# Performance work log

Hardware: AMD Instinct MI355X
Metric: run time of the kernel (lower is better)

## Reference

```python
import jax, jax.numpy as jnp
import numpy as np

S = 256          # fine grid extent (active region within full_scale=4096)
SC = S // 2      # coarse grid extent after stride-2 downsample
N = 400_000      # active fine voxels
C_IN, M0, M1 = 3, 32, 64   # input features; unet_structure = [32, 64]
NCLASS = 20
EPS = 1e-4       # scn.BatchNormReLU default eps


def _build_nbr(keys_sorted, coords, s):
    """27-neighborhood index table for a sparse voxel set (hash via sorted keys)."""
    n = coords.shape[0]
    nbr = np.full((n, 27), -1, dtype=np.int32)
    x, y, z = coords[:, 0], coords[:, 1], coords[:, 2]
    k = 0
    for dx in (-1, 0, 1):
        for dy in (-1, 0, 1):
            for dz in (-1, 0, 1):
                nx, ny, nz = x + dx, y + dy, z + dz
                valid = (nx >= 0) & (nx < s) & (ny >= 0) & (ny < s) & (nz >= 0) & (nz < s)
                ck = (nx.astype(np.int64) * s + ny) * s + nz
                pos = np.clip(np.searchsorted(keys_sorted, ck), 0, n - 1)
                nbr[:, k] = np.where(valid & (keys_sorted[pos] == ck), pos, -1)
                k += 1
    return nbr


def setup_inputs() -> dict:
    rng = np.random.default_rng(0)
    keys = np.sort(rng.choice(S ** 3, size=N, replace=False).astype(np.int64))
    x = keys // (S * S); y = (keys // S) % S; z = keys % S
    coords = np.stack([x, y, z], 1)
    nbr_fine = _build_nbr(keys, coords, S)
    # stride-2 pooling structure
    ckeys = ((x // 2) * SC + (y // 2)) * SC + (z // 2)
    uk, parent_id = np.unique(ckeys, return_inverse=True)
    ccoords = np.stack([uk // (SC * SC), (uk // SC) % SC, uk % SC], 1)
    nbr_coarse = _build_nbr(uk, ccoords, SC)
    child_off = ((x & 1) * 4 + (y & 1) * 2 + (z & 1)).astype(np.int32)

    ks = jax.random.split(jax.random.key(0), 16)
    def w(k, shape, fan_in):
        return jax.random.normal(k, shape, jnp.float32) * (1.0 / np.sqrt(fan_in))
    return {
        "feats": jax.random.normal(ks[0], (N, C_IN), jnp.float32),
        "nbr_fine": jnp.asarray(nbr_fine),
        "nbr_coarse": jnp.asarray(nbr_coarse),
        "parent_id": jnp.asarray(parent_id.astype(np.int32)),
        "child_off": jnp.asarray(child_off),
        "W_sub": w(ks[1], (27, C_IN, M0), 27 * C_IN),
        "W_e0": w(ks[2], (27, M0, M0), 27 * M0),
        "g0": jnp.ones((M0,), jnp.float32), "b0": jnp.zeros((M0,), jnp.float32),
        "W_down": w(ks[3], (8, M0, M1), 8 * M0),
        "W_e1": w(ks[4], (27, M1, M1), 27 * M1),
        "g1": jnp.ones((M1,), jnp.float32), "b1": jnp.zeros((M1,), jnp.float32),
        "W_up": w(ks[5], (8, M1, M0), 8 * M1),
        "W_dec": w(ks[6], (27, 2 * M0, M0), 27 * 2 * M0),
        "g_out": jnp.ones((M0,), jnp.float32), "b_out": jnp.zeros((M0,), jnp.float32),
        "W_lin": w(ks[7], (M0, NCLASS), M0),
        "b_lin": jnp.zeros((NCLASS,), jnp.float32),
    }


def _subconv(feat, nbr, W):
    """Submanifold 3x3x3 conv: fixed loop over 27 kernel taps (gather+GEMM)."""
    out = jnp.zeros((feat.shape[0], W.shape[2]), feat.dtype)
    for k in range(27):
        idx = nbr[:, k]
        g = jnp.where(idx[:, None] >= 0, feat[jnp.clip(idx, 0)], 0.0)
        out = out + g @ W[k]
    return out


def _bnrelu(xv, g, b):
    mu = xv.mean(0)
    var = xv.var(0)
    return jax.nn.relu((xv - mu) * jax.lax.rsqrt(var + EPS) * g + b)


def reference(feats, nbr_fine, nbr_coarse, parent_id, child_off,
              W_sub, W_e0, g0, b0, W_down, W_e1, g1, b1, W_up, W_dec,
              g_out, b_out, W_lin, b_lin):
    M = nbr_coarse.shape[0]
    xv = _subconv(feats, nbr_fine, W_sub)                       # [N, M0]
    e0 = _bnrelu(_subconv(xv, nbr_fine, W_e0), g0, b0)          # encoder level 0
    # stride-2 sparse conv (scatter-add children into parents, per-offset weight)
    down = jax.ops.segment_sum(jnp.einsum('nc,ncd->nd', e0, W_down[child_off]),
                               parent_id, num_segments=M)        # [M, M1]
    e1 = _bnrelu(_subconv(down, nbr_coarse, W_e1), g1, b1)      # encoder level 1
    # stride-2 sparse deconv (gather parent, per-offset weight)
    up = jnp.einsum('nc,ncd->nd', e1[parent_id], W_up[child_off])  # [N, M0]
    dec = _subconv(jnp.concatenate([e0, up], 1), nbr_fine, W_dec)  # decoder join
    feature = _bnrelu(dec, g_out, b_out)                        # final BatchNormReLU
    y = feature @ W_lin + b_lin                                 # class head
    return (y, feature)
```

## Files before the change

kernel.cpp:

```cpp
#include <hip/hip_runtime.h>
#include <hip/hip_bf16.h>

#define BN_EPS 1e-4f

typedef __attribute__((ext_vector_type(8))) short short8;
typedef __attribute__((ext_vector_type(4))) float float4e;

__device__ __forceinline__ int rfl(int x) { return __builtin_amdgcn_readfirstlane(x); }

__device__ __forceinline__ float ldf(const __hip_bfloat16* p) { return __bfloat162float(*p); }
__device__ __forceinline__ void stf(__hip_bfloat16* p, float v) { *p = __float2bfloat16(v); }

__device__ __forceinline__ short bfbits(float x) {
    __hip_bfloat16 h = __float2bfloat16(x);
    short s;
    __builtin_memcpy(&s, &h, 2);
    return s;
}
__device__ __forceinline__ short8 cvt8(float4 a, float4 b) {
    short8 r;
    r[0] = bfbits(a.x); r[1] = bfbits(a.y); r[2] = bfbits(a.z); r[3] = bfbits(a.w);
    r[4] = bfbits(b.x); r[5] = bfbits(b.y); r[6] = bfbits(b.z); r[7] = bfbits(b.w);
    return r;
}

__global__ __launch_bounds__(256) void k_pack(const float* __restrict__ src,
                                              __hip_bfloat16* __restrict__ dst,
                                              int CIN, int COUT, int KT, int NT, int total) {
    int i = blockIdx.x * 256 + threadIdx.x;
    if (i >= total) return;
    int j = i & 7, lane = (i >> 3) & 63;
    int g = i >> 9;
    int nt = g % NT; g /= NT;
    int kt = g % KT; g /= KT;
    int t = g;
    int q = lane >> 4, c = lane & 15;
    dst[i] = __float2bfloat16(src[((size_t)t * CIN + kt * 32 + q * 8 + j) * COUT + nt * 16 + c]);
}

__global__ __launch_bounds__(256) void k_xv(const float* __restrict__ feats,
                                            const int* __restrict__ nbr,
                                            const float* __restrict__ W,
                                            __hip_bfloat16* __restrict__ out, int N) {
    int n = blockIdx.x * 256 + threadIdx.x;
    if (n >= N) return;
    float acc[32];
#pragma unroll
    for (int d = 0; d < 32; ++d) acc[d] = 0.f;
    const int* nb = nbr + (size_t)n * 27;
    for (int k = 0; k < 27; ++k) {
        int idx = nb[k];
        if (idx < 0) continue;
        float f0 = feats[(size_t)idx * 3 + 0];
        float f1 = feats[(size_t)idx * 3 + 1];
        float f2 = feats[(size_t)idx * 3 + 2];
        const float* w = W + k * 96;
#pragma unroll
        for (int d = 0; d < 32; ++d)
            acc[d] += f0 * w[d] + f1 * w[32 + d] + f2 * w[64 + d];
    }
    short8* o = (short8*)(out + (size_t)n * 32);
#pragma unroll
    for (int c = 0; c < 4; ++c) {
        short8 r;
#pragma unroll
        for (int j = 0; j < 8; ++j) r[j] = bfbits(acc[c * 8 + j]);
        o[c] = r;
    }
}

template <int CIN, int COUT, int MODE>
__global__ __launch_bounds__(256, 4) void k_conv(const void* __restrict__ inAv,
                                                 const void* __restrict__ inBv,
                                                 const int* __restrict__ nbr,
                                                 const __hip_bfloat16* __restrict__ Wp,
                                                 __hip_bfloat16* __restrict__ out,
                                                 int nrows,
                                                 float* __restrict__ ssum,
                                                 float* __restrict__ ssq) {
    constexpr int KT = CIN / 32;
    constexpr int NT = COUT / 16;
    __shared__ int sidx[4][432];
    const __hip_bfloat16* inAb = (const __hip_bfloat16*)inAv;
    const __hip_bfloat16* inBb = (const __hip_bfloat16*)inBv;
    const float* inAf = (const float*)inAv;
    const int tid = threadIdx.x;
    const int lane = tid & 63;
    const int wv = tid >> 6;
    const int m15 = lane & 15;
    const int q = lane >> 4;
    int* my = sidx[wv];
    int wid = blockIdx.x * 4 + wv;
    int nw = gridDim.x * 4;
    const int ntile = (nrows + 15) / 16;
    float sS[NT], sQ[NT];
#pragma unroll
    for (int nt = 0; nt < NT; ++nt) { sS[nt] = 0.f; sQ[nt] = 0.f; }

    for (int tile = wid; tile < ntile; tile += nw) {
        const int row0 = rfl(tile) * 16;
        int nr = nrows - row0;
        nr = nr > 16 ? 16 : nr;
        const int* src = nbr + (size_t)row0 * 27;
        const int tot = nr * 27;
        for (int t = lane; t < 432; t += 64) {
            int v = -1;
            if (t < tot) v = src[t];
            int r = t / 27;
            my[(t - r * 27) * 16 + r] = v;
        }
        float4e acc[NT];
#pragma unroll
        for (int nt = 0; nt < NT; ++nt) acc[nt] = (float4e)0.f;

        short8 gs[KT], gs2[KT];
        float4 gf[4], gf2[4];
        auto load_g = [&](int ir, short8 g[KT], float4 f[4]) {
            size_t id = (size_t)(ir < 0 ? 0 : ir);
            if (MODE == 0) {
                g[0] = *(const short8*)(inAb + id * 32 + q * 8);
            } else if (MODE == 2) {
                g[0] = *(const short8*)(inAb + id * 32 + q * 8);
                g[1] = *(const short8*)(inBb + id * 32 + q * 8);
            } else {
                const float* b = inAf + id * 64 + q * 8;
                f[0] = *(const float4*)(b);
                f[1] = *(const float4*)(b + 4);
                f[2] = *(const float4*)(b + 32);
                f[3] = *(const float4*)(b + 36);
            }
        };

        int irA = my[m15];
        int irB = my[16 + m15];
        int mA = rfl((int)(__ballot(irA >= 0) & 0xffff));
        if (mA) load_g(irA, gs, gf);
        for (int k = 0; k < 27; ++k) {
            int mB = rfl((int)(__ballot(irB >= 0) & 0xffff));
            int irC = -1;
            if (k + 2 < 27) irC = my[(k + 2) * 16 + m15];
            if (mB) load_g(irB, gs2, gf2);
            if (mA) {
                short8 a[KT];
                if (MODE == 1) {
                    a[0] = cvt8(gf[0], gf[1]);
                    a[1] = cvt8(gf[2], gf[3]);
                } else {
#pragma unroll
                    for (int kt = 0; kt < KT; ++kt) a[kt] = gs[kt];
                }
                short8 z = (short8)(short)0;
#pragma unroll
                for (int kt = 0; kt < KT; ++kt) a[kt] = (irA >= 0) ? a[kt] : z;
                const short8* bp = (const short8*)Wp + (size_t)k * KT * NT * 64 + lane;
#pragma unroll
                for (int nt = 0; nt < NT; ++nt) {
#pragma unroll
                    for (int kt = 0; kt < KT; ++kt) {
                        short8 b = bp[(kt * NT + nt) * 64];
                        acc[nt] = __builtin_amdgcn_mfma_f32_16x16x32_bf16(a[kt], b, acc[nt], 0, 0, 0);
                    }
                }
            }
            mA = mB; irA = irB; irB = irC;
#pragma unroll
            for (int kt = 0; kt < KT; ++kt) gs[kt] = gs2[kt];
            if (MODE == 1) {
#pragma unroll
                for (int i = 0; i < 4; ++i) gf[i] = gf2[i];
            }
        }
#pragma unroll
        for (int nt = 0; nt < NT; ++nt) {
#pragma unroll
            for (int r = 0; r < 4; ++r) {
                int rowg = row0 + q * 4 + r;
                if (rowg < nrows) {
                    float v = acc[nt][r];
                    stf(out + (size_t)rowg * COUT + nt * 16 + m15, v);
                    sS[nt] += v;
                    sQ[nt] += v * v;
                }
            }
        }
    }
#pragma unroll
    for (int nt = 0; nt < NT; ++nt) {
        float v = sS[nt], w = sQ[nt];
        v += __shfl_xor(v, 16); v += __shfl_xor(v, 32);
        w += __shfl_xor(w, 16); w += __shfl_xor(w, 32);
        if (lane < 16) {
            atomicAdd(&ssum[nt * 16 + lane], v);
            atomicAdd(&ssq[nt * 16 + lane], w);
        }
    }
}

__global__ void k_fin(const float* __restrict__ ssum, const float* __restrict__ ssq,
                      const float* __restrict__ g, const float* __restrict__ b,
                      float* __restrict__ scale, float* __restrict__ shift,
                      int C, float invN) {
    int c = blockIdx.x * blockDim.x + threadIdx.x;
    if (c >= C) return;
    float mu = ssum[c] * invN;
    float var = fmaxf(ssq[c] * invN - mu * mu, 0.f);
    float s = g[c] * rsqrtf(var + BN_EPS);
    scale[c] = s;
    shift[c] = b[c] - mu * s;
}

__global__ __launch_bounds__(256) void k_down(__hip_bfloat16* __restrict__ e0,
                                              const int* __restrict__ parent,
                                              const int* __restrict__ child,
                                              const float* __restrict__ Wd,
                                              const float* __restrict__ sc,
                                              const float* __restrict__ sh,
                                              float* __restrict__ down, int N) {
    const int lane = threadIdx.x & 63;
    int wid = blockIdx.x * 4 + (threadIdx.x >> 6);
    int nw = gridDim.x * 4;
    for (int row = wid; row < N; row += nw) {
        int urow = rfl(row);
        float v = 0.f;
        if (lane < 32) {
            float r = ldf(e0 + (size_t)urow * 32 + lane);
            v = fmaxf(fmaf(r, sc[lane], sh[lane]), 0.f);
            stf(e0 + (size_t)urow * 32 + lane, v);
        }
        int par = rfl(parent[urow]);
        int off = rfl(child[urow]);
        float acc = 0.f;
        const float* wb = Wd + (size_t)off * 2048 + lane;
#pragma unroll
        for (int c = 0; c < 32; ++c)
            acc = fmaf(__shfl(v, c), wb[c * 64], acc);
        atomicAdd(&down[(size_t)par * 64 + lane], acc);
    }
}

__global__ __launch_bounds__(256) void k_up(const __hip_bfloat16* __restrict__ e1raw,
                                            const int* __restrict__ parent,
                                            const int* __restrict__ child,
                                            const float* __restrict__ Wu,
                                            const float* __restrict__ sc,
                                            const float* __restrict__ sh,
                                            __hip_bfloat16* __restrict__ up, int N) {
    const int lane = threadIdx.x & 63;
    int wid = blockIdx.x * 4 + (threadIdx.x >> 6);
    int nw = gridDim.x * 4;
    for (int row = wid; row < N; row += nw) {
        int urow = rfl(row);
        int par = rfl(parent[urow]);
        int off = rfl(child[urow]);
        float e = ldf(e1raw + (size_t)par * 64 + lane);
        float v = fmaxf(fmaf(e, sc[lane], sh[lane]), 0.f);
        int d = lane & 31, hi = lane >> 5;
        float acc = 0.f;
        const float* wb = Wu + (size_t)off * 2048 + (size_t)hi * 1024 + d;
#pragma unroll
        for (int c = 0; c < 32; ++c)
            acc = fmaf(__shfl(v, hi * 32 + c), wb[c * 32], acc);
        acc += __shfl_xor(acc, 32);
        if (hi == 0) stf(up + (size_t)urow * 32 + d, acc);
    }
}

__global__ __launch_bounds__(256) void k_out(const __hip_bfloat16* __restrict__ dec,
                                             const float* __restrict__ sc,
                                             const float* __restrict__ sh,
                                             const float* __restrict__ Wl,
                                             const float* __restrict__ bl,
                                             float* __restrict__ y,
                                             float* __restrict__ feat, int N) {
    int n = blockIdx.x * 256 + threadIdx.x;
    if (n >= N) return;
    float f[32];
    const __hip_bfloat162* p = (const __hip_bfloat162*)(dec + (size_t)n * 32);
#pragma unroll
    for (int j = 0; j < 16; ++j) {
        float2 t = __bfloat1622float2(p[j]);
        f[2 * j + 0] = fmaxf(fmaf(t.x, sc[2 * j + 0], sh[2 * j + 0]), 0.f);
        f[2 * j + 1] = fmaxf(fmaf(t.y, sc[2 * j + 1], sh[2 * j + 1]), 0.f);
    }
    float4* fo = (float4*)(feat + (size_t)n * 32);
#pragma unroll
    for (int j = 0; j < 8; ++j)
        fo[j] = make_float4(f[4 * j], f[4 * j + 1], f[4 * j + 2], f[4 * j + 3]);
    float acc[20];
#pragma unroll
    for (int qq = 0; qq < 20; ++qq) acc[qq] = bl[qq];
#pragma unroll
    for (int c = 0; c < 32; ++c) {
        float fc = f[c];
#pragma unroll
        for (int qq = 0; qq < 20; ++qq) acc[qq] = fmaf(fc, Wl[c * 20 + qq], acc[qq]);
    }
    float4* yo = (float4*)(y + (size_t)n * 20);
#pragma unroll
    for (int j = 0; j < 5; ++j)
        yo[j] = make_float4(acc[4 * j], acc[4 * j + 1], acc[4 * j + 2], acc[4 * j + 3]);
}

extern "C" void kernel_launch(void* const* d_in, const int* in_sizes, int n_in,
                              void* d_out, int out_size, void* d_ws, size_t ws_size,
                              hipStream_t stream) {
    const float* feats = (const float*)d_in[0];
    const int* nbr_f   = (const int*)d_in[1];
    const int* nbr_c   = (const int*)d_in[2];
    const int* parent  = (const int*)d_in[3];
    const int* child   = (const int*)d_in[4];
    const float* W_sub = (const float*)d_in[5];
    const float* W_e0  = (const float*)d_in[6];
    const float* g0    = (const float*)d_in[7];
    const float* b0    = (const float*)d_in[8];
    const float* W_dn  = (const float*)d_in[9];
    const float* W_e1  = (const float*)d_in[10];
    const float* g1    = (const float*)d_in[11];
    const float* b1    = (const float*)d_in[12];
    const float* W_up  = (const float*)d_in[13];
    const float* W_dec = (const float*)d_in[14];
    const float* g_o   = (const float*)d_in[15];
    const float* b_o   = (const float*)d_in[16];
    const float* W_lin = (const float*)d_in[17];
    const float* b_lin = (const float*)d_in[18];

    const int N = in_sizes[0] / 3;
    const int M = in_sizes[2] / 27;

    float* wsf = (float*)d_ws;
    size_t R = (size_t)M * 64;
    if ((size_t)N * 32 > R) R = (size_t)N * 32;
    __hip_bfloat16* xvb = (__hip_bfloat16*)wsf;
    float* down = wsf;
    __hip_bfloat16* up     = (__hip_bfloat16*)wsf;
    __hip_bfloat16* decraw = (__hip_bfloat16*)(wsf + (size_t)N * 16);
    float* stats = wsf + R;

    __hip_bfloat16* e0    = (__hip_bfloat16*)d_out;
    __hip_bfloat16* e1raw = (__hip_bfloat16*)((float*)d_out + (size_t)N * 16);
    __hip_bfloat16* Wp0   = (__hip_bfloat16*)((float*)d_out + (size_t)N * 16 + (size_t)M * 32);
    const int T0 = 27 * 1 * 2 * 512;
    const int T1 = 27 * 2 * 4 * 512;
    const int T2 = 27 * 2 * 2 * 512;
    __hip_bfloat16* Wp1 = Wp0 + T0;
    __hip_bfloat16* Wp2 = Wp1 + T1;
    float* y    = (float*)d_out;
    float* feat = y + (size_t)N * 20;

    const int nblk = (N + 255) / 256;
    const int G = 2048;

    hipMemsetAsync(stats, 0, 256 * sizeof(float), stream);
    k_pack<<<(T0 + 255) / 256, 256, 0, stream>>>(W_e0, Wp0, 32, 32, 1, 2, T0);
    k_pack<<<(T1 + 255) / 256, 256, 0, stream>>>(W_e1, Wp1, 64, 64, 2, 4, T1);
    k_pack<<<(T2 + 255) / 256, 256, 0, stream>>>(W_dec, Wp2, 64, 32, 2, 2, T2);

    k_xv<<<nblk, 256, 0, stream>>>(feats, nbr_f, W_sub, xvb, N);
    k_conv<32, 32, 0><<<G, 256, 0, stream>>>(xvb, nullptr, nbr_f, Wp0, e0, N,
                                             stats + 0, stats + 32);
    hipMemsetAsync(down, 0, (size_t)M * 64 * sizeof(float), stream);
    k_fin<<<1, 64, 0, stream>>>(stats + 0, stats + 32, g0, b0,
                                stats + 256, stats + 288, 32, 1.f / (float)N);
    k_down<<<G, 256, 0, stream>>>(e0, parent, child, W_dn,
                                  stats + 256, stats + 288, down, N);
    k_conv<64, 64, 1><<<G, 256, 0, stream>>>(down, nullptr, nbr_c, Wp1, e1raw, M,
                                             stats + 64, stats + 128);
    k_fin<<<1, 64, 0, stream>>>(stats + 64, stats + 128, g1, b1,
                                stats + 320, stats + 384, 64, 1.f / (float)M);
    k_up<<<G, 256, 0, stream>>>(e1raw, parent, child, W_up,
                                stats + 320, stats + 384, up, N);
    k_conv<64, 32, 2><<<G, 256, 0, stream>>>(e0, up, nbr_f, Wp2, decraw, N,
                                             stats + 192, stats + 224);
    k_fin<<<1, 64, 0, stream>>>(stats + 192, stats + 224, g_o, b_o,
                                stats + 448, stats + 480, 32, 1.f / (float)N);
    k_out<<<nblk, 256, 0, stream>>>(decraw, stats + 448, stats + 480, W_lin, b_lin,
                                    y, feat, N);
}
```

Measured before the change: 1.692 ms.

## Deepen gather prefetch, add atomic tile scheduler, pre-convert coarse features to bf16

The sparse conv kernel now keeps PD neighbour gathers in flight (8 for e0, 5 for the others) instead of double-buffering, to hide more gather latency. Static grid-stride tile assignment is replaced by per-wave atomic work-stealing on counters placed in the stats scratch region. The neighbour table is copied into LDS without the transpose. For the coarse conv, the fp32 down buffer is first converted to bf16 by a new kernel, so the conv gathers half the bytes and skips per-offset conversion; there is a fallback if workspace is too small. Deeper prefetch raises register pressure and may reduce occupancy, and the atomics add a little contention.

```diff
diff --git a/kernel.cpp b/kernel.cpp
--- a/kernel.cpp
+++ b/kernel.cpp
@@ -69,7 +69,16 @@
     }
 }
 
-template <int CIN, int COUT, int MODE>
+__global__ __launch_bounds__(256) void k_cvt(const float* __restrict__ src,
+                                             __hip_bfloat16* __restrict__ dst, int n8) {
+    int i = blockIdx.x * 256 + threadIdx.x;
+    if (i >= n8) return;
+    const float4* p = (const float4*)src + (size_t)i * 2;
+    float4 a = p[0], b = p[1];
+    ((short8*)dst)[i] = cvt8(a, b);
+}
+
+template <int CIN, int COUT, int MODE, int PD>
 __global__ __launch_bounds__(256, 4) void k_conv(const void* __restrict__ inAv,
                                                  const void* __restrict__ inBv,
                                                  const int* __restrict__ nbr,
@@ -77,7 +86,8 @@
                                                  __hip_bfloat16* __restrict__ out,
                                                  int nrows,
                                                  float* __restrict__ ssum,
-                                                 float* __restrict__ ssq) {
+                                                 float* __restrict__ ssq,
+                                                 int* __restrict__ ctr) {
     constexpr int KT = CIN / 32;
     constexpr int NT = COUT / 16;
     __shared__ int sidx[4][432];
@@ -90,68 +100,68 @@
     const int m15 = lane & 15;
     const int q = lane >> 4;
     int* my = sidx[wv];
-    int wid = blockIdx.x * 4 + wv;
-    int nw = gridDim.x * 4;
     const int ntile = (nrows + 15) / 16;
     float sS[NT], sQ[NT];
 #pragma unroll
     for (int nt = 0; nt < NT; ++nt) { sS[nt] = 0.f; sQ[nt] = 0.f; }
 
-    for (int tile = wid; tile < ntile; tile += nw) {
-        const int row0 = rfl(tile) * 16;
+    for (;;) {
+        int tg = 0;
+        if (lane == 0) tg = atomicAdd(ctr, 1);
+        const int tile = rfl(tg);
+        if (tile >= ntile) break;
+        const int row0 = tile * 16;
         int nr = nrows - row0;
         nr = nr > 16 ? 16 : nr;
         const int* src = nbr + (size_t)row0 * 27;
         const int tot = nr * 27;
-        for (int t = lane; t < 432; t += 64) {
-            int v = -1;
-            if (t < tot) v = src[t];
-            int r = t / 27;
-            my[(t - r * 27) * 16 + r] = v;
-        }
+        for (int t = lane; t < 432; t += 64) my[t] = (t < tot) ? src[t] : -1;
         float4e acc[NT];
 #pragma unroll
         for (int nt = 0; nt < NT; ++nt) acc[nt] = (float4e)0.f;
 
-        short8 gs[KT], gs2[KT];
-        float4 gf[4], gf2[4];
-        auto load_g = [&](int ir, short8 g[KT], float4 f[4]) {
-            size_t id = (size_t)(ir < 0 ? 0 : ir);
-            if (MODE == 0) {
-                g[0] = *(const short8*)(inAb + id * 32 + q * 8);
-            } else if (MODE == 2) {
-                g[0] = *(const short8*)(inAb + id * 32 + q * 8);
-                g[1] = *(const short8*)(inBb + id * 32 + q * 8);
+        int ir[PD], mk[PD];
+        short8 g[PD][KT];
+        float4 gf[PD][4];
+        auto load_g = [&](int idxv, short8* gg, float4* ff) {
+            size_t id = (size_t)(idxv < 0 ? 0 : idxv);
+            if constexpr (MODE == 1) {
+                const float* b = inAf + id * 64 + q * 8;
+                ff[0] = *(const float4*)(b);
+                ff[1] = *(const float4*)(b + 4);
+                ff[2] = *(const float4*)(b + 32);
+                ff[3] = *(const float4*)(b + 36);
+            } else if constexpr (MODE == 2) {
+                gg[0] = *(const short8*)(inAb + id * 32 + q * 8);
+                gg[1] = *(const short8*)(inBb + id * 32 + q * 8);
             } else {
-                const float* b = inAf + id * 64 + q * 8;
-                f[0] = *(const float4*)(b);
-                f[1] = *(const float4*)(b + 4);
-                f[2] = *(const float4*)(b + 32);
-                f[3] = *(const float4*)(b + 36);
+#pragma unroll
+                for (int kt = 0; kt < KT; ++kt)
+                    gg[kt] = *(const short8*)(inAb + id * CIN + kt * 32 + q * 8);
             }
         };
 
-        int irA = my[m15];
-        int irB = my[16 + m15];
-        int mA = rfl((int)(__ballot(irA >= 0) & 0xffff));
-        if (mA) load_g(irA, gs, gf);
+#pragma unroll
+        for (int d = 0; d < PD; ++d) {
+            ir[d] = my[m15 * 27 + d];
+            mk[d] = rfl((int)(__ballot(ir[d] >= 0) & 0xffff));
+            load_g(ir[d], g[d], gf[d]);
+        }
+#pragma unroll
         for (int k = 0; k < 27; ++k) {
-            int mB = rfl((int)(__ballot(irB >= 0) & 0xffff));
-            int irC = -1;
-            if (k + 2 < 27) irC = my[(k + 2) * 16 + m15];
-            if (mB) load_g(irB, gs2, gf2);
-            if (mA) {
+            const int s = k % PD;
+            if (mk[s]) {
                 short8 a[KT];
-                if (MODE == 1) {
-                    a[0] = cvt8(gf[0], gf[1]);
-                    a[1] = cvt8(gf[2], gf[3]);
+                if constexpr (MODE == 1) {
+                    a[0] = cvt8(gf[s][0], gf[s][1]);
+                    a[1] = cvt8(gf[s][2], gf[s][3]);
                 } else {
 #pragma unroll
-                    for (int kt = 0; kt < KT; ++kt) a[kt] = gs[kt];
+                    for (int kt = 0; kt < KT; ++kt) a[kt] = g[s][kt];
                 }
                 short8 z = (short8)(short)0;
 #pragma unroll
-                for (int kt = 0; kt < KT; ++kt) a[kt] = (irA >= 0) ? a[kt] : z;
+                for (int kt = 0; kt < KT; ++kt) a[kt] = (ir[s] >= 0) ? a[kt] : z;
                 const short8* bp = (const short8*)Wp + (size_t)k * KT * NT * 64 + lane;
 #pragma unroll
                 for (int nt = 0; nt < NT; ++nt) {
@@ -162,12 +172,10 @@
                     }
                 }
             }
-            mA = mB; irA = irB; irB = irC;
-#pragma unroll
-            for (int kt = 0; kt < KT; ++kt) gs[kt] = gs2[kt];
-            if (MODE == 1) {
-#pragma unroll
-                for (int i = 0; i < 4; ++i) gf[i] = gf2[i];
+            if (k + PD < 27) {
+                ir[s] = my[m15 * 27 + (k + PD)];
+                mk[s] = rfl((int)(__ballot(ir[s] >= 0) & 0xffff));
+                load_g(ir[s], g[s], gf[s]);
             }
         }
 #pragma unroll
@@ -335,6 +343,9 @@
     __hip_bfloat16* up     = (__hip_bfloat16*)wsf;
     __hip_bfloat16* decraw = (__hip_bfloat16*)(wsf + (size_t)N * 16);
     float* stats = wsf + R;
+    int* c_e0  = (int*)(stats + 256);
+    int* c_e1  = (int*)(stats + 448);
+    int* c_dec = (int*)(stats + 449);
 
     __hip_bfloat16* e0    = (__hip_bfloat16*)d_out;
     __hip_bfloat16* e1raw = (__hip_bfloat16*)((float*)d_out + (size_t)N * 16);
@@ -350,27 +361,38 @@
     const int nblk = (N + 255) / 256;
     const int G = 2048;
 
-    hipMemsetAsync(stats, 0, 256 * sizeof(float), stream);
+    hipMemsetAsync(stats, 0, 512 * sizeof(float), stream);
     k_pack<<<(T0 + 255) / 256, 256, 0, stream>>>(W_e0, Wp0, 32, 32, 1, 2, T0);
     k_pack<<<(T1 + 255) / 256, 256, 0, stream>>>(W_e1, Wp1, 64, 64, 2, 4, T1);
     k_pack<<<(T2 + 255) / 256, 256, 0, stream>>>(W_dec, Wp2, 64, 32, 2, 2, T2);
 
     k_xv<<<nblk, 256, 0, stream>>>(feats, nbr_f, W_sub, xvb, N);
-    k_conv<32, 32, 0><<<G, 256, 0, stream>>>(xvb, nullptr, nbr_f, Wp0, e0, N,
-                                             stats + 0, stats + 32);
+    k_conv<32, 32, 0, 8><<<G, 256, 0, stream>>>(xvb, nullptr, nbr_f, Wp0, e0, N,
+                                                stats + 0, stats + 32, c_e0);
     hipMemsetAsync(down, 0, (size_t)M * 64 * sizeof(float), stream);
     k_fin<<<1, 64, 0, stream>>>(stats + 0, stats + 32, g0, b0,
                                 stats + 256, stats + 288, 32, 1.f / (float)N);
     k_down<<<G, 256, 0, stream>>>(e0, parent, child, W_dn,
                                   stats + 256, stats + 288, down, N);
-    k_conv<64, 64, 1><<<G, 256, 0, stream>>>(down, nullptr, nbr_c, Wp1, e1raw, M,
-                                             stats + 64, stats + 128);
+    {
+        size_t base = (R + 512) * sizeof(float);
+        size_t needb = base + (size_t)M * 64 * sizeof(__hip_bfloat16);
+        if (ws_size >= needb) {
+            __hip_bfloat16* downb = (__hip_bfloat16*)((char*)d_ws + base);
+            k_cvt<<<((M * 8) + 255) / 256, 256, 0, stream>>>(down, downb, M * 8);
+            k_conv<64, 64, 0, 5><<<G, 256, 0, stream>>>(downb, nullptr, nbr_c, Wp1, e1raw, M,
+                                                        stats + 64, stats + 128, c_e1);
+        } else {
+            k_conv<64, 64, 1, 2><<<G, 256, 0, stream>>>(down, nullptr, nbr_c, Wp1, e1raw, M,
+                                                        stats + 64, stats + 128, c_e1);
+        }
+    }
     k_fin<<<1, 64, 0, stream>>>(stats + 64, stats + 128, g1, b1,
                                 stats + 320, stats + 384, 64, 1.f / (float)M);
     k_up<<<G, 256, 0, stream>>>(e1raw, parent, child, W_up,
                                 stats + 320, stats + 384, up, N);
-    k_conv<64, 32, 2><<<G, 256, 0, stream>>>(e0, up, nbr_f, Wp2, decraw, N,
-                                             stats + 192, stats + 224);
+    k_conv<64, 32, 2, 5><<<G, 256, 0, stream>>>(e0, up, nbr_f, Wp2, decraw, N,
+                                                stats + 192, stats + 224, c_dec);
     k_fin<<<1, 64, 0, stream>>>(stats + 192, stats + 224, g_o, b_o,
                                 stats + 448, stats + 480, 32, 1.f / (float)N);
     k_out<<<nblk, 256, 0, stream>>>(decraw, stats + 448, stats + 480, W_lin, b_lin,
```

After: 2.999 ms. 77.2% more time.

## Use atomic work-stealing tiles in sparse conv and pre-convert coarse input to bf16

Applied to the files above, without the earlier changes.

The sparse conv kernel replaces its static grid-stride tile assignment with a global atomic counter, so each wave grabs the next 16-row tile dynamically and load imbalance shrinks. The neighbor index tile is now copied into shared memory in row-major order without the transpose, and reads use a stride-27 index instead. The coarse-level conv gets a small kernel that converts the fp32 `down` buffer to bf16 first, so it can use the bf16 gather path instead of converting fp32 inside the inner loop. This costs an extra kernel launch, extra workspace, and one atomic per tile, and the counters share the stats buffer, which adds an ordering risk.

```diff
diff --git a/kernel.cpp b/kernel.cpp
--- a/kernel.cpp
+++ b/kernel.cpp
@@ -69,6 +69,15 @@
     }
 }
 
+__global__ __launch_bounds__(256) void k_cvt(const float* __restrict__ src,
+                                             __hip_bfloat16* __restrict__ dst, int n8) {
+    int i = blockIdx.x * 256 + threadIdx.x;
+    if (i >= n8) return;
+    const float4* p = (const float4*)src + (size_t)i * 2;
+    float4 a = p[0], b = p[1];
+    ((short8*)dst)[i] = cvt8(a, b);
+}
+
 template <int CIN, int COUT, int MODE>
 __global__ __launch_bounds__(256, 4) void k_conv(const void* __restrict__ inAv,
                                                  const void* __restrict__ inBv,
@@ -77,7 +86,8 @@
                                                  __hip_bfloat16* __restrict__ out,
                                                  int nrows,
                                                  float* __restrict__ ssum,
-                                                 float* __restrict__ ssq) {
+                                                 float* __restrict__ ssq,
+                                                 int* __restrict__ ctr) {
     constexpr int KT = CIN / 32;
     constexpr int NT = COUT / 16;
     __shared__ int sidx[4][432];
@@ -90,25 +100,22 @@
     const int m15 = lane & 15;
     const int q = lane >> 4;
     int* my = sidx[wv];
-    int wid = blockIdx.x * 4 + wv;
-    int nw = gridDim.x * 4;
     const int ntile = (nrows + 15) / 16;
     float sS[NT], sQ[NT];
 #pragma unroll
     for (int nt = 0; nt < NT; ++nt) { sS[nt] = 0.f; sQ[nt] = 0.f; }
 
-    for (int tile = wid; tile < ntile; tile += nw) {
-        const int row0 = rfl(tile) * 16;
+    for (;;) {
+        int tg = 0;
+        if (lane == 0) tg = atomicAdd(ctr, 1);
+        const int tile = rfl(tg);
+        if (tile >= ntile) break;
+        const int row0 = tile * 16;
         int nr = nrows - row0;
         nr = nr > 16 ? 16 : nr;
         const int* src = nbr + (size_t)row0 * 27;
         const int tot = nr * 27;
-        for (int t = lane; t < 432; t += 64) {
-            int v = -1;
-            if (t < tot) v = src[t];
-            int r = t / 27;
-            my[(t - r * 27) * 16 + r] = v;
-        }
+        for (int t = lane; t < 432; t += 64) my[t] = (t < tot) ? src[t] : -1;
         float4e acc[NT];
 #pragma unroll
         for (int nt = 0; nt < NT; ++nt) acc[nt] = (float4e)0.f;
@@ -118,7 +125,9 @@
         auto load_g = [&](int ir, short8 g[KT], float4 f[4]) {
             size_t id = (size_t)(ir < 0 ? 0 : ir);
             if (MODE == 0) {
-                g[0] = *(const short8*)(inAb + id * 32 + q * 8);
+#pragma unroll
+                for (int kt = 0; kt < KT; ++kt)
+                    g[kt] = *(const short8*)(inAb + id * CIN + kt * 32 + q * 8);
             } else if (MODE == 2) {
                 g[0] = *(const short8*)(inAb + id * 32 + q * 8);
                 g[1] = *(const short8*)(inBb + id * 32 + q * 8);
@@ -131,14 +140,14 @@
             }
         };
 
-        int irA = my[m15];
-        int irB = my[16 + m15];
+        int irA = my[m15 * 27 + 0];
+        int irB = my[m15 * 27 + 1];
         int mA = rfl((int)(__ballot(irA >= 0) & 0xffff));
         if (mA) load_g(irA, gs, gf);
         for (int k = 0; k < 27; ++k) {
             int mB = rfl((int)(__ballot(irB >= 0) & 0xffff));
             int irC = -1;
-            if (k + 2 < 27) irC = my[(k + 2) * 16 + m15];
+            if (k + 2 < 27) irC = my[m15 * 27 + (k + 2)];
             if (mB) load_g(irB, gs2, gf2);
             if (mA) {
                 short8 a[KT];
@@ -335,6 +344,9 @@
     __hip_bfloat16* up     = (__hip_bfloat16*)wsf;
     __hip_bfloat16* decraw = (__hip_bfloat16*)(wsf + (size_t)N * 16);
     float* stats = wsf + R;
+    int* c_e0  = (int*)(stats + 256);
+    int* c_e1  = (int*)(stats + 448);
+    int* c_dec = (int*)(stats + 449);
 
     __hip_bfloat16* e0    = (__hip_bfloat16*)d_out;
     __hip_bfloat16* e1raw = (__hip_bfloat16*)((float*)d_out + (size_t)N * 16);
@@ -350,27 +362,38 @@
     const int nblk = (N + 255) / 256;
     const int G = 2048;
 
-    hipMemsetAsync(stats, 0, 256 * sizeof(float), stream);
+    hipMemsetAsync(stats, 0, 512 * sizeof(float), stream);
     k_pack<<<(T0 + 255) / 256, 256, 0, stream>>>(W_e0, Wp0, 32, 32, 1, 2, T0);
     k_pack<<<(T1 + 255) / 256, 256, 0, stream>>>(W_e1, Wp1, 64, 64, 2, 4, T1);
     k_pack<<<(T2 + 255) / 256, 256, 0, stream>>>(W_dec, Wp2, 64, 32, 2, 2, T2);
 
     k_xv<<<nblk, 256, 0, stream>>>(feats, nbr_f, W_sub, xvb, N);
     k_conv<32, 32, 0><<<G, 256, 0, stream>>>(xvb, nullptr, nbr_f, Wp0, e0, N,
-                                             stats + 0, stats + 32);
+                                             stats + 0, stats + 32, c_e0);
     hipMemsetAsync(down, 0, (size_t)M * 64 * sizeof(float), stream);
     k_fin<<<1, 64, 0, stream>>>(stats + 0, stats + 32, g0, b0,
                                 stats + 256, stats + 288, 32, 1.f / (float)N);
     k_down<<<G, 256, 0, stream>>>(e0, parent, child, W_dn,
                                   stats + 256, stats + 288, down, N);
-    k_conv<64, 64, 1><<<G, 256, 0, stream>>>(down, nullptr, nbr_c, Wp1, e1raw, M,
-                                             stats + 64, stats + 128);
+    {
+        size_t base = (R + 512) * sizeof(float);
+        size_t needb = base + (size_t)M * 64 * sizeof(__hip_bfloat16);
+        if (ws_size >= needb) {
+            __hip_bfloat16* downb = (__hip_bfloat16*)((char*)d_ws + base);
+            k_cvt<<<((M * 8) + 255) / 256, 256, 0, stream>>>(down, downb, M * 8);
+            k_conv<64, 64, 0><<<G, 256, 0, stream>>>(downb, nullptr, nbr_c, Wp1, e1raw, M,
+                                                     stats + 64, stats + 128, c_e1);
+        } else {
+            k_conv<64, 64, 1><<<G, 256, 0, stream>>>(down, nullptr, nbr_c, Wp1, e1raw, M,
+                                                     stats + 64, stats + 128, c_e1);
+        }
+    }
     k_fin<<<1, 64, 0, stream>>>(stats + 64, stats + 128, g1, b1,
                                 stats + 320, stats + 384, 64, 1.f / (float)M);
     k_up<<<G, 256, 0, stream>>>(e1raw, parent, child, W_up,
                                 stats + 320, stats + 384, up, N);
     k_conv<64, 32, 2><<<G, 256, 0, stream>>>(e0, up, nbr_f, Wp2, decraw, N,
-                                             stats + 192, stats + 224);
+                                             stats + 192, stats + 224, c_dec);
     k_fin<<<1, 64, 0, stream>>>(stats + 192, stats + 224, g_o, b_o,
                                 stats + 448, stats + 480, 32, 1.f / (float)N);
     k_out<<<nblk, 256, 0, stream>>>(decraw, stats + 448, stats + 480, W_lin, b_lin,
```

Result: slower. 2.964 ms (+75.2%).
